# Performance work log

Hardware: AMD Instinct MI355X
Metric: run time of the kernel (lower is better)

## Reference

```python
import jax, jax.numpy as jnp
import numpy as np

B, N, DIM = 16, 1024, 768


def setup_inputs() -> dict:
    key = jax.random.key(0)
    ks = jax.random.split(key, 8)
    x = jax.random.normal(ks[0], (B, N, DIM), dtype=jnp.float32)
    y = jax.random.normal(ks[1], (B, N, DIM), dtype=jnp.float32)
    coords = jax.random.normal(ks[2], (N, N, 6), dtype=jnp.float32)
    # orthogonal init for U (as in torch init.orthogonal_)
    a = jax.random.normal(ks[3], (DIM, DIM), dtype=jnp.float32)
    q, r = jnp.linalg.qr(a)
    U = q * jnp.sign(jnp.diagonal(r))[None, :]
    S1 = jnp.ones((DIM,), dtype=jnp.float32)
    S2 = jnp.ones((DIM,), dtype=jnp.float32)
    gating = jnp.asarray(1.0, dtype=jnp.float32)
    temp = jnp.asarray(0.1, dtype=jnp.float32)
    pos_emb = jnp.zeros((N, 6, 1), dtype=jnp.float32)
    return {"x": x, "y": y, "coords": coords, "U": U, "S1": S1, "S2": S2,
            "gating": gating, "temp": temp, "pos_emb": pos_emb}


def reference(x, y, coords, U, S1, S2, gating, temp, pos_emb):
    dim = x.shape[-1]
    scale = dim ** (-0.5)
    # spectral decomposition: x @ U^T @ diag(S^2) @ U
    xu = x @ U.T                                   # [B,N,d]
    x1 = (xu * jnp.square(S1)) @ U                 # [B,N,d]
    x2 = (xu * jnp.square(S2)) @ U                 # [B,N,d]
    xs = jnp.stack([x1, x2], axis=1)               # [B,2,N,d]
    patch_score = jax.nn.softmax(
        jnp.einsum('bknd,bmd->bknm', xs, y) * scale, axis=-1)  # [B,2,N,M]
    pos = jnp.squeeze(coords @ pos_emb, -1)        # [N,M]
    pos_score = jax.nn.softmax(pos, axis=-1)[None, None]        # [1,1,N,M]
    g = jax.nn.sigmoid(gating)
    attn = (1.0 - g) * patch_score + g * pos_score  # [B,2,N,M]
    # entropy-routed gating
    entropy = jnp.sum(-attn * jnp.log(attn + 1e-8), axis=-1)    # [B,2,N]
    hmap = 2.0 - 2.0 * jax.nn.sigmoid(temp * jnp.transpose(entropy, (0, 2, 1)))  # [B,N,2]
    fgbg = hmap[..., 0] >= hmap[..., 1]
    route = jax.lax.stop_gradient(
        jnp.stack([fgbg, ~fgbg], axis=-1).astype(hmap.dtype))   # [B,N,2]
    heat_map = jnp.sum(hmap * route, axis=-1, keepdims=True)    # [B,N,1]
    attn_c = jnp.sum(attn * jnp.transpose(route, (0, 2, 1))[..., None], axis=1)  # [B,N,M]
    out = attn_c @ y                               # [B,N,d]
    return (out, heat_map)
```

## Files before the change

### kernel.cpp

```cpp
#include <hip/hip_runtime.h>
#include <hip/hip_bf16.h>

#define DEV __device__ __forceinline__

typedef unsigned short u16;
typedef short short8 __attribute__((ext_vector_type(8)));
typedef float f32x4 __attribute__((ext_vector_type(4)));

static const int BB = 16;
static const int NN = 1024;
static const int DD = 768;

DEV u16 f2bf(float f) {
    unsigned u = __builtin_bit_cast(unsigned, f);
    unsigned r = u + 0x7fffu + ((u >> 16) & 1u);
    return (u16)(r >> 16);
}
DEV float h2f(u16 u) { return (float)__builtin_bit_cast(_Float16, u); }
DEV u16 f2h(float f) { return __builtin_bit_cast(u16, (_Float16)f); }

DEV short8 ldf8_bf(const float* p) {
    float4 f0 = *(const float4*)p;
    float4 f1 = *(const float4*)(p + 4);
    short8 r;
    r[0] = (short)f2bf(f0.x); r[1] = (short)f2bf(f0.y);
    r[2] = (short)f2bf(f0.z); r[3] = (short)f2bf(f0.w);
    r[4] = (short)f2bf(f1.x); r[5] = (short)f2bf(f1.y);
    r[6] = (short)f2bf(f1.z); r[7] = (short)f2bf(f1.w);
    return r;
}

DEV void gl_lds16(const u16* g, u16* l) {
    __builtin_amdgcn_global_load_lds(
        (const __attribute__((address_space(1))) unsigned int*)g,
        (__attribute__((address_space(3))) unsigned int*)l, 16, 0, 0);
}

template<int OM>
__global__ __launch_bounds__(256) void gemm128(
    const u16* __restrict__ Ag, const u16* __restrict__ Bg, void* __restrict__ Cg,
    int K, int N, int zmod,
    long sA0, long sA1, long sB0, long sB1, long sC0, long sC1,
    float scale)
{
    __shared__ u16 As[128 * 64];
    __shared__ u16 Bs[128 * 64];

    int z = blockIdx.z;
    const u16* A = Ag + (long)(z % zmod) * sA0 + (long)(z / zmod) * sA1;
    const u16* B = Bg + (long)(z % zmod) * sB0 + (long)(z / zmod) * sB1;
    u16*   Cu = (u16*)Cg   + (long)(z % zmod) * sC0 + (long)(z / zmod) * sC1;
    float* Cf = (float*)Cg + (long)(z % zmod) * sC0 + (long)(z / zmod) * sC1;

    int tid  = threadIdx.x;
    int lane = tid & 63, wave = tid >> 6;
    int wm = wave & 1, wn = wave >> 1;
    int lr = lane & 15, quad = lane >> 4;

    long m0 = (long)blockIdx.x * 128;
    long n0 = (long)blockIdx.y * 128;

    long aOfs[4], bOfs[4];
    u16 *lA[4], *lB[4];
#pragma unroll
    for (int i = 0; i < 4; i++) {
        int p = tid + i * 256;
        int row = p >> 3, qs = p & 7;
        int q = qs ^ (row & 7);
        aOfs[i] = (m0 + row) * (long)K + q * 8;
        bOfs[i] = (n0 + row) * (long)K + q * 8;
        lA[i] = As + p * 8;
        lB[i] = Bs + p * 8;
    }

    int aoff[4][2], boff[4][2];
#pragma unroll
    for (int t = 0; t < 4; t++) {
        int ra = wm * 64 + t * 16 + lr;
        int rb = wn * 64 + t * 16 + lr;
#pragma unroll
        for (int h = 0; h < 2; h++) {
            aoff[t][h] = ra * 64 + (((h * 4 + quad) ^ (ra & 7)) * 8);
            boff[t][h] = rb * 64 + (((h * 4 + quad) ^ (rb & 7)) * 8);
        }
    }

    f32x4 acc[4][4] = {};

    for (int k0 = 0; k0 < K; k0 += 64) {
#pragma unroll
        for (int i = 0; i < 4; i++) gl_lds16(A + aOfs[i] + k0, lA[i]);
#pragma unroll
        for (int i = 0; i < 4; i++) gl_lds16(B + bOfs[i] + k0, lB[i]);
        __syncthreads();

#pragma unroll
        for (int h = 0; h < 2; h++) {
            short8 af[4], bfr[4];
#pragma unroll
            for (int t = 0; t < 4; t++) af[t]  = *(const short8*)(As + aoff[t][h]);
#pragma unroll
            for (int t = 0; t < 4; t++) bfr[t] = *(const short8*)(Bs + boff[t][h]);
#pragma unroll
            for (int ti = 0; ti < 4; ti++)
#pragma unroll
                for (int tj = 0; tj < 4; tj++)
                    acc[ti][tj] = __builtin_amdgcn_mfma_f32_16x16x32_bf16(
                        af[ti], bfr[tj], acc[ti][tj], 0, 0, 0);
        }
        __syncthreads();
    }

    long crow = m0 + wm * 64 + quad * 4;
    long ccol = n0 + wn * 64 + lr;
#pragma unroll
    for (int ti = 0; ti < 4; ti++)
#pragma unroll
        for (int tj = 0; tj < 4; tj++)
#pragma unroll
            for (int r = 0; r < 4; r++) {
                long row = crow + ti * 16 + r;
                long col = ccol + tj * 16;
                float v = acc[ti][tj][r] * scale;
                long idx = row * (long)N + col;
                if constexpr (OM == 0)      Cu[idx] = f2bf(v);
                else if constexpr (OM == 1) Cu[idx] = f2h(v);
                else                        Cf[idx] = v;
            }
}

__global__ __launch_bounds__(256) void k_prep_u(
    const float* __restrict__ U, const float* __restrict__ S1,
    const float* __restrict__ S2, u16* __restrict__ UTb,
    u16* __restrict__ VT1, u16* __restrict__ VT2)
{
    __shared__ float tile[32][33];
    int i0 = blockIdx.x * 32, j0 = blockIdx.y * 32;
#pragma unroll
    for (int r = 0; r < 32; r += 8) {
        int i = i0 + threadIdx.y + r, j = j0 + threadIdx.x;
        tile[threadIdx.y + r][threadIdx.x] = U[(long)i * DD + j];
    }
    __syncthreads();
    float s1v = S1[i0 + threadIdx.x];
    float s2v = S2[i0 + threadIdx.x];
    s1v *= s1v; s2v *= s2v;
#pragma unroll
    for (int r = 0; r < 32; r += 8) {
        int j = j0 + threadIdx.y + r, i = i0 + threadIdx.x;
        float v = tile[threadIdx.x][threadIdx.y + r];
        UTb[(long)j * DD + i] = f2bf(v);
        VT1[(long)j * DD + i] = f2bf(s1v * v);
        VT2[(long)j * DD + i] = f2bf(s2v * v);
    }
}

__global__ __launch_bounds__(256) void k_conv_x(
    const float* __restrict__ x, u16* __restrict__ xb)
{
    long i = ((long)blockIdx.x * 256 + threadIdx.x) * 8;
    *(short8*)(xb + i) = ldf8_bf(x + i);
}

__global__ __launch_bounds__(256) void k_conv_y(
    const float* __restrict__ y, u16* __restrict__ yb, u16* __restrict__ yT)
{
    __shared__ float tile[32][33];
    int b = blockIdx.z;
    int d0 = blockIdx.x * 32, m0 = blockIdx.y * 32;
    const float* ybase = y + (long)b * NN * DD;
#pragma unroll
    for (int r = 0; r < 32; r += 8) {
        int m = m0 + threadIdx.y + r, d = d0 + threadIdx.x;
        float v = ybase[(long)m * DD + d];
        tile[threadIdx.y + r][threadIdx.x] = v;
        yb[(long)b * NN * DD + (long)m * DD + d] = f2bf(v);
    }
    __syncthreads();
#pragma unroll
    for (int r = 0; r < 32; r += 8) {
        int d = d0 + threadIdx.y + r, m = m0 + threadIdx.x;
        yT[(long)b * DD * NN + (long)d * NN + m] = f2bf(tile[threadIdx.x][threadIdx.y + r]);
    }
}

DEV float wave_red_max(float v) {
#pragma unroll
    for (int o = 32; o; o >>= 1) v = fmaxf(v, __shfl_xor(v, o));
    return v;
}
DEV float wave_red_sum(float v) {
#pragma unroll
    for (int o = 32; o; o >>= 1) v += __shfl_xor(v, o);
    return v;
}
DEV float block_red_max(float v, float* sh) {
    v = wave_red_max(v);
    if ((threadIdx.x & 63) == 0) sh[threadIdx.x >> 6] = v;
    __syncthreads();
    v = fmaxf(fmaxf(sh[0], sh[1]), fmaxf(sh[2], sh[3]));
    __syncthreads();
    return v;
}
DEV float block_red_sum(float v, float* sh) {
    v = wave_red_sum(v);
    if ((threadIdx.x & 63) == 0) sh[threadIdx.x >> 6] = v;
    __syncthreads();
    v = (sh[0] + sh[1]) + (sh[2] + sh[3]);
    __syncthreads();
    return v;
}

__global__ __launch_bounds__(256) void k_pos(
    const float* __restrict__ coords, const float* __restrict__ pe,
    float* __restrict__ P)
{
    __shared__ float sh[4];
    int n = blockIdx.x, t = threadIdx.x;
    float p6[6];
#pragma unroll
    for (int c = 0; c < 6; c++) p6[c] = pe[n * 6 + c];
    float v[4];
#pragma unroll
    for (int i = 0; i < 4; i++) {
        const float* cp = coords + ((long)n * NN + t * 4 + i) * 6;
        v[i] = p6[0]*cp[0] + p6[1]*cp[1] + p6[2]*cp[2] + p6[3]*cp[3] + p6[4]*cp[4] + p6[5]*cp[5];
    }
    float mx = block_red_max(fmaxf(fmaxf(v[0], v[1]), fmaxf(v[2], v[3])), sh);
    float e[4], s = 0.f;
#pragma unroll
    for (int i = 0; i < 4; i++) { e[i] = expf(v[i] - mx); s += e[i]; }
    float Z = block_red_sum(s, sh);
    float inv = 1.f / Z;
    float4 o; o.x = e[0]*inv; o.y = e[1]*inv; o.z = e[2]*inv; o.w = e[3]*inv;
    *(float4*)(P + ((long)n << 10) + t * 4) = o;
}

__global__ __launch_bounds__(256) void k_route(
    u16* __restrict__ S, const float* __restrict__ P,
    const float* __restrict__ gating, const float* __restrict__ temp,
    float* __restrict__ heat)
{
    __shared__ float sh[4];
    int bn = blockIdx.x;
    int b = bn >> 10, n = bn & 1023, t = threadIdx.x;
    u16* s1p = S + ((long)(b * 2) << 20) + ((long)n << 10) + t * 4;
    u16* s2p = s1p + (1L << 20);
    const float* pp = P + ((long)n << 10) + t * 4;

    ushort4 r1 = *(const ushort4*)s1p;
    ushort4 r2 = *(const ushort4*)s2p;
    float4 pv = *(const float4*)pp;
    float s1[4] = { h2f(r1.x), h2f(r1.y), h2f(r1.z), h2f(r1.w) };
    float s2[4] = { h2f(r2.x), h2f(r2.y), h2f(r2.z), h2f(r2.w) };
    float p4[4] = { pv.x, pv.y, pv.z, pv.w };

    float mx1 = block_red_max(fmaxf(fmaxf(s1[0], s1[1]), fmaxf(s1[2], s1[3])), sh);
    float mx2 = block_red_max(fmaxf(fmaxf(s2[0], s2[1]), fmaxf(s2[2], s2[3])), sh);

    float e1[4], e2[4], z1 = 0.f, z2 = 0.f;
#pragma unroll
    for (int i = 0; i < 4; i++) {
        e1[i] = expf(s1[i] - mx1); z1 += e1[i];
        e2[i] = expf(s2[i] - mx2); z2 += e2[i];
    }
    float Z1 = block_red_sum(z1, sh);
    float Z2 = block_red_sum(z2, sh);

    float g = 1.f / (1.f + expf(-gating[0]));
    float c1 = (1.f - g) / Z1, c2 = (1.f - g) / Z2;

    float a1[4], a2[4], hh1 = 0.f, hh2 = 0.f;
#pragma unroll
    for (int i = 0; i < 4; i++) {
        a1[i] = e1[i] * c1 + g * p4[i];
        a2[i] = e2[i] * c2 + g * p4[i];
        hh1 -= a1[i] * logf(a1[i] + 1e-8f);
        hh2 -= a2[i] * logf(a2[i] + 1e-8f);
    }
    float H1 = block_red_sum(hh1, sh);
    float H2 = block_red_sum(hh2, sh);

    float tv = temp[0];
    float hm0 = 2.f - 2.f / (1.f + expf(-tv * H1));
    float hm1 = 2.f - 2.f / (1.f + expf(-tv * H2));
    int ks = (hm0 >= hm1) ? 0 : 1;
    if (t == 0) heat[bn] = ks ? hm1 : hm0;

    ushort4 w;
    w.x = f2bf(ks ? a2[0] : a1[0]);
    w.y = f2bf(ks ? a2[1] : a1[1]);
    w.z = f2bf(ks ? a2[2] : a1[2]);
    w.w = f2bf(ks ? a2[3] : a1[3]);
    *(ushort4*)s1p = w;
}

extern "C" void kernel_launch(void* const* d_in, const int* in_sizes, int n_in,
                              void* d_out, int out_size, void* d_ws, size_t ws_size,
                              hipStream_t stream)
{
    (void)in_sizes; (void)n_in; (void)out_size; (void)ws_size;
    const float* x      = (const float*)d_in[0];
    const float* y      = (const float*)d_in[1];
    const float* coords = (const float*)d_in[2];
    const float* U      = (const float*)d_in[3];
    const float* S1     = (const float*)d_in[4];
    const float* S2     = (const float*)d_in[5];
    const float* gating = (const float*)d_in[6];
    const float* temp   = (const float*)d_in[7];
    const float* pose   = (const float*)d_in[8];

    float* out  = (float*)d_out;
    float* heat = out + (long)BB * NN * DD;

    char* w = (char*)d_ws;
    u16* UTb = (u16*)w;  w += (long)DD * DD * 2;
    u16* VT  = (u16*)w;  w += (long)2 * DD * DD * 2;
    u16* W2  = (u16*)w;  w += (long)2 * DD * DD * 2;
    u16* xb  = (u16*)w;  w += (long)BB * NN * DD * 2;
    u16* x12 = (u16*)w;  w += (long)2 * BB * NN * DD * 2;
    u16* yb  = (u16*)w;  w += (long)BB * NN * DD * 2;
    u16* yT  = (u16*)w;  w += (long)BB * DD * NN * 2;
    u16* S   = (u16*)w;  w += (long)BB * 2 * NN * NN * 2;
    float* P = (float*)w;

    const long MBN = (long)BB * NN * DD;
    const long BND = (long)NN * DD;
    const long SPL = (long)NN * NN;
    const long DSQ = (long)DD * DD;

    k_prep_u<<<dim3(24, 24), dim3(32, 8), 0, stream>>>(U, S1, S2, UTb, VT, VT + DSQ);
    k_conv_x<<<dim3(MBN / 2048), dim3(256), 0, stream>>>(x, xb);
    k_conv_y<<<dim3(DD / 32, NN / 32, BB), dim3(32, 8), 0, stream>>>(y, yb, yT);
    k_pos<<<dim3(NN), dim3(256), 0, stream>>>(coords, pose, P);

    gemm128<0><<<dim3(DD / 128, DD / 128, 2), dim3(256), 0, stream>>>(
        UTb, VT, W2, DD, DD, 2,
        0L, 0L, DSQ, 0L, DSQ, 0L, 1.0f);

    gemm128<0><<<dim3(BB * NN / 128, DD / 128, 2), dim3(256), 0, stream>>>(
        xb, W2, x12, DD, DD, 2,
        0L, 0L, DSQ, 0L, MBN, 0L, 1.0f);

    gemm128<1><<<dim3(NN / 128, NN / 128, BB * 2), dim3(256), 0, stream>>>(
        x12, yb, S, DD, NN, 2,
        MBN, BND, 0L, BND, SPL, 2 * SPL, 0.036084391824351615f);

    k_route<<<dim3(BB * NN), dim3(256), 0, stream>>>(S, P, gating, temp, heat);

    gemm128<2><<<dim3(NN / 128, DD / 128, BB), dim3(256), 0, stream>>>(
        S, yT, out, NN, DD, 1,
        0L, 2 * SPL, 0L, BND, 0L, BND, 1.0f);
}
```

Measured before the change: 400.2 us.

## Use 32x32x16 MFMA tiles in GEMM and fuse prep kernels into one launch

The GEMM now uses the 32x32x16 bf16 MFMA with 2x2 accumulator tiles per wave instead of 4x4 tiles of 16x16x32. This issues fewer MFMA instructions and LDS fragment loads per k-step, and it changes the output store pattern. Launch bounds now request 3 blocks per SIMD-level occupancy. The four preprocessing kernels (x convert, y convert/transpose, positional softmax, U prep) are merged into one kernel that dispatches on block index, which removes launch overhead and lets the independent work overlap.

After: 384.6 us. 3.9% less time.

```diff
diff --git a/kernel.cpp b/kernel.cpp
--- a/kernel.cpp
+++ b/kernel.cpp
@@ -5,7 +5,7 @@
 
 typedef unsigned short u16;
 typedef short short8 __attribute__((ext_vector_type(8)));
-typedef float f32x4 __attribute__((ext_vector_type(4)));
+typedef float f32x16 __attribute__((ext_vector_type(16)));
 
 static const int BB = 16;
 static const int NN = 1024;
@@ -37,7 +37,7 @@
 }
 
 template<int OM>
-__global__ __launch_bounds__(256) void gemm128(
+__global__ __launch_bounds__(256, 3) void gemm128(
     const u16* __restrict__ Ag, const u16* __restrict__ Bg, void* __restrict__ Cg,
     int K, int N, int zmod,
     long sA0, long sA1, long sB0, long sB1, long sC0, long sC1,
@@ -55,7 +55,7 @@
     int tid  = threadIdx.x;
     int lane = tid & 63, wave = tid >> 6;
     int wm = wave & 1, wn = wave >> 1;
-    int lr = lane & 15, quad = lane >> 4;
+    int ln31 = lane & 31, khalf = lane >> 5;
 
     long m0 = (long)blockIdx.x * 128;
     long n0 = (long)blockIdx.y * 128;
@@ -73,19 +73,19 @@
         lB[i] = Bs + p * 8;
     }
 
-    int aoff[4][2], boff[4][2];
-#pragma unroll
-    for (int t = 0; t < 4; t++) {
-        int ra = wm * 64 + t * 16 + lr;
-        int rb = wn * 64 + t * 16 + lr;
-#pragma unroll
-        for (int h = 0; h < 2; h++) {
-            aoff[t][h] = ra * 64 + (((h * 4 + quad) ^ (ra & 7)) * 8);
-            boff[t][h] = rb * 64 + (((h * 4 + quad) ^ (rb & 7)) * 8);
-        }
-    }
-
-    f32x4 acc[4][4] = {};
+    int aoff[2][4], boff[2][4];
+#pragma unroll
+    for (int t = 0; t < 2; t++) {
+        int ra = wm * 64 + t * 32 + ln31;
+        int rb = wn * 64 + t * 32 + ln31;
+#pragma unroll
+        for (int h = 0; h < 4; h++) {
+            aoff[t][h] = ra * 64 + (((h * 2 + khalf) ^ (ra & 7)) * 8);
+            boff[t][h] = rb * 64 + (((h * 2 + khalf) ^ (rb & 7)) * 8);
+        }
+    }
+
+    f32x16 acc[2][2] = {};
 
     for (int k0 = 0; k0 < K; k0 += 64) {
 #pragma unroll
@@ -95,93 +95,38 @@
         __syncthreads();
 
 #pragma unroll
-        for (int h = 0; h < 2; h++) {
-            short8 af[4], bfr[4];
-#pragma unroll
-            for (int t = 0; t < 4; t++) af[t]  = *(const short8*)(As + aoff[t][h]);
-#pragma unroll
-            for (int t = 0; t < 4; t++) bfr[t] = *(const short8*)(Bs + boff[t][h]);
-#pragma unroll
-            for (int ti = 0; ti < 4; ti++)
-#pragma unroll
-                for (int tj = 0; tj < 4; tj++)
-                    acc[ti][tj] = __builtin_amdgcn_mfma_f32_16x16x32_bf16(
+        for (int h = 0; h < 4; h++) {
+            short8 af[2], bfr[2];
+#pragma unroll
+            for (int t = 0; t < 2; t++) af[t]  = *(const short8*)(As + aoff[t][h]);
+#pragma unroll
+            for (int t = 0; t < 2; t++) bfr[t] = *(const short8*)(Bs + boff[t][h]);
+#pragma unroll
+            for (int ti = 0; ti < 2; ti++)
+#pragma unroll
+                for (int tj = 0; tj < 2; tj++)
+                    acc[ti][tj] = __builtin_amdgcn_mfma_f32_32x32x16_bf16(
                         af[ti], bfr[tj], acc[ti][tj], 0, 0, 0);
         }
         __syncthreads();
     }
 
-    long crow = m0 + wm * 64 + quad * 4;
-    long ccol = n0 + wn * 64 + lr;
-#pragma unroll
-    for (int ti = 0; ti < 4; ti++)
-#pragma unroll
-        for (int tj = 0; tj < 4; tj++)
-#pragma unroll
-            for (int r = 0; r < 4; r++) {
-                long row = crow + ti * 16 + r;
-                long col = ccol + tj * 16;
+    long crow = m0 + wm * 64 + 4 * khalf;
+    long ccol = n0 + wn * 64 + ln31;
+#pragma unroll
+    for (int ti = 0; ti < 2; ti++)
+#pragma unroll
+        for (int tj = 0; tj < 2; tj++)
+#pragma unroll
+            for (int r = 0; r < 16; r++) {
+                long row = crow + ti * 32 + (r & 3) + 8 * (r >> 2);
+                long col = ccol + tj * 32;
                 float v = acc[ti][tj][r] * scale;
                 long idx = row * (long)N + col;
                 if constexpr (OM == 0)      Cu[idx] = f2bf(v);
                 else if constexpr (OM == 1) Cu[idx] = f2h(v);
                 else                        Cf[idx] = v;
             }
-}
-
-__global__ __launch_bounds__(256) void k_prep_u(
-    const float* __restrict__ U, const float* __restrict__ S1,
-    const float* __restrict__ S2, u16* __restrict__ UTb,
-    u16* __restrict__ VT1, u16* __restrict__ VT2)
-{
-    __shared__ float tile[32][33];
-    int i0 = blockIdx.x * 32, j0 = blockIdx.y * 32;
-#pragma unroll
-    for (int r = 0; r < 32; r += 8) {
-        int i = i0 + threadIdx.y + r, j = j0 + threadIdx.x;
-        tile[threadIdx.y + r][threadIdx.x] = U[(long)i * DD + j];
-    }
-    __syncthreads();
-    float s1v = S1[i0 + threadIdx.x];
-    float s2v = S2[i0 + threadIdx.x];
-    s1v *= s1v; s2v *= s2v;
-#pragma unroll
-    for (int r = 0; r < 32; r += 8) {
-        int j = j0 + threadIdx.y + r, i = i0 + threadIdx.x;
-        float v = tile[threadIdx.x][threadIdx.y + r];
-        UTb[(long)j * DD + i] = f2bf(v);
-        VT1[(long)j * DD + i] = f2bf(s1v * v);
-        VT2[(long)j * DD + i] = f2bf(s2v * v);
-    }
-}
-
-__global__ __launch_bounds__(256) void k_conv_x(
-    const float* __restrict__ x, u16* __restrict__ xb)
-{
-    long i = ((long)blockIdx.x * 256 + threadIdx.x) * 8;
-    *(short8*)(xb + i) = ldf8_bf(x + i);
-}
-
-__global__ __launch_bounds__(256) void k_conv_y(
-    const float* __restrict__ y, u16* __restrict__ yb, u16* __restrict__ yT)
-{
-    __shared__ float tile[32][33];
-    int b = blockIdx.z;
-    int d0 = blockIdx.x * 32, m0 = blockIdx.y * 32;
-    const float* ybase = y + (long)b * NN * DD;
-#pragma unroll
-    for (int r = 0; r < 32; r += 8) {
-        int m = m0 + threadIdx.y + r, d = d0 + threadIdx.x;
-        float v = ybase[(long)m * DD + d];
-        tile[threadIdx.y + r][threadIdx.x] = v;
-        yb[(long)b * NN * DD + (long)m * DD + d] = f2bf(v);
-    }
-    __syncthreads();
-#pragma unroll
-    for (int r = 0; r < 32; r += 8) {
-        int d = d0 + threadIdx.y + r, m = m0 + threadIdx.x;
-        yT[(long)b * DD * NN + (long)d * NN + m] = f2bf(tile[threadIdx.x][threadIdx.y + r]);
-    }
 }
 
 DEV float wave_red_max(float v) {
@@ -211,29 +156,94 @@
     return v;
 }
 
-__global__ __launch_bounds__(256) void k_pos(
-    const float* __restrict__ coords, const float* __restrict__ pe,
+__global__ __launch_bounds__(256) void k_prep_all(
+    const float* __restrict__ x, const float* __restrict__ y,
+    const float* __restrict__ coords, const float* __restrict__ U,
+    const float* __restrict__ S1, const float* __restrict__ S2,
+    const float* __restrict__ pe,
+    u16* __restrict__ xb, u16* __restrict__ yb, u16* __restrict__ yT,
+    u16* __restrict__ UTb, u16* __restrict__ VT1, u16* __restrict__ VT2,
     float* __restrict__ P)
 {
-    __shared__ float sh[4];
-    int n = blockIdx.x, t = threadIdx.x;
-    float p6[6];
-#pragma unroll
-    for (int c = 0; c < 6; c++) p6[c] = pe[n * 6 + c];
-    float v[4];
-#pragma unroll
-    for (int i = 0; i < 4; i++) {
-        const float* cp = coords + ((long)n * NN + t * 4 + i) * 6;
-        v[i] = p6[0]*cp[0] + p6[1]*cp[1] + p6[2]*cp[2] + p6[3]*cp[3] + p6[4]*cp[4] + p6[5]*cp[5];
-    }
-    float mx = block_red_max(fmaxf(fmaxf(v[0], v[1]), fmaxf(v[2], v[3])), sh);
-    float e[4], s = 0.f;
-#pragma unroll
-    for (int i = 0; i < 4; i++) { e[i] = expf(v[i] - mx); s += e[i]; }
-    float Z = block_red_sum(s, sh);
-    float inv = 1.f / Z;
-    float4 o; o.x = e[0]*inv; o.y = e[1]*inv; o.z = e[2]*inv; o.w = e[3]*inv;
-    *(float4*)(P + ((long)n << 10) + t * 4) = o;
+    __shared__ float shmem[32 * 33];
+    int bid = blockIdx.x, tid = threadIdx.x;
+
+    if (bid < 6144) {
+        long i = ((long)bid * 256 + tid) * 8;
+        *(short8*)(xb + i) = ldf8_bf(x + i);
+        return;
+    }
+    bid -= 6144;
+
+    if (bid < 12288) {
+        float (*tile)[33] = (float(*)[33])shmem;
+        int b = bid / 768, rem = bid % 768;
+        int d0 = (rem % 24) * 32, m0 = (rem / 24) * 32;
+        int tx = tid & 31, ty = tid >> 5;
+        const float* ybase = y + (long)b * NN * DD;
+#pragma unroll
+        for (int r = 0; r < 32; r += 8) {
+            int m = m0 + ty + r, d = d0 + tx;
+            float v = ybase[(long)m * DD + d];
+            tile[ty + r][tx] = v;
+            yb[(long)b * NN * DD + (long)m * DD + d] = f2bf(v);
+        }
+        __syncthreads();
+#pragma unroll
+        for (int r = 0; r < 32; r += 8) {
+            int d = d0 + ty + r, m = m0 + tx;
+            yT[(long)b * DD * NN + (long)d * NN + m] = f2bf(tile[tx][ty + r]);
+        }
+        return;
+    }
+    bid -= 12288;
+
+    if (bid < 1024) {
+        int n = bid, t = tid;
+        float p6[6];
+#pragma unroll
+        for (int c = 0; c < 6; c++) p6[c] = pe[n * 6 + c];
+        float v[4];
+#pragma unroll
+        for (int i = 0; i < 4; i++) {
+            const float* cp = coords + ((long)n * NN + t * 4 + i) * 6;
+            v[i] = p6[0]*cp[0] + p6[1]*cp[1] + p6[2]*cp[2]
+                 + p6[3]*cp[3] + p6[4]*cp[4] + p6[5]*cp[5];
+        }
+        float mx = block_red_max(fmaxf(fmaxf(v[0], v[1]), fmaxf(v[2], v[3])), shmem);
+        float e[4], s = 0.f;
+#pragma unroll
+        for (int i = 0; i < 4; i++) { e[i] = expf(v[i] - mx); s += e[i]; }
+        float Z = block_red_sum(s, shmem);
+        float inv = 1.f / Z;
+        float4 o; o.x = e[0]*inv; o.y = e[1]*inv; o.z = e[2]*inv; o.w = e[3]*inv;
+        *(float4*)(P + ((long)n << 10) + t * 4) = o;
+        return;
+    }
+    bid -= 1024;
+
+    {
+        float (*tile)[33] = (float(*)[33])shmem;
+        int i0 = (bid % 24) * 32, j0 = (bid / 24) * 32;
+        int tx = tid & 31, ty = tid >> 5;
+#pragma unroll
+        for (int r = 0; r < 32; r += 8) {
+            int i = i0 + ty + r, j = j0 + tx;
+            tile[ty + r][tx] = U[(long)i * DD + j];
+        }
+        __syncthreads();
+        float s1v = S1[i0 + tx];
+        float s2v = S2[i0 + tx];
+        s1v *= s1v; s2v *= s2v;
+#pragma unroll
+        for (int r = 0; r < 32; r += 8) {
+            int j = j0 + ty + r, i = i0 + tx;
+            float v = tile[tx][ty + r];
+            UTb[(long)j * DD + i] = f2bf(v);
+            VT1[(long)j * DD + i] = f2bf(s1v * v);
+            VT2[(long)j * DD + i] = f2bf(s2v * v);
+        }
+    }
 }
 
 __global__ __launch_bounds__(256) void k_route(
@@ -329,10 +339,8 @@
     const long SPL = (long)NN * NN;
     const long DSQ = (long)DD * DD;
 
-    k_prep_u<<<dim3(24, 24), dim3(32, 8), 0, stream>>>(U, S1, S2, UTb, VT, VT + DSQ);
-    k_conv_x<<<dim3(MBN / 2048), dim3(256), 0, stream>>>(x, xb);
-    k_conv_y<<<dim3(DD / 32, NN / 32, BB), dim3(32, 8), 0, stream>>>(y, yb, yT);
-    k_pos<<<dim3(NN), dim3(256), 0, stream>>>(coords, pose, P);
+    k_prep_all<<<dim3(20032), dim3(256), 0, stream>>>(
+        x, y, coords, U, S1, S2, pose, xb, yb, yT, UTb, VT, VT + DSQ, P);
 
     gemm128<0><<<dim3(DD / 128, DD / 128, 2), dim3(256), 0, stream>>>(
         UTb, VT, W2, DD, DD, 2,
```
